# Optimization experiments

Measured on AMD Instinct MI355X. Metric: run time of the kernel, lower is better.

Reference implementation:

```python
import jax, jax.numpy as jnp
import numpy as np

B, L, D = 4, 1024, 256
N_PER, N_HYP = 48, 16  # n_oscillators=64, n_hyperbolic=16
K = N_PER + N_HYP


def _mlp(x, w1, b1, w2, b2):
    # torch nn.Linear: y = x @ W.T + b; GELU is exact (erf) by default
    h = jax.nn.gelu(x @ w1.T + b1, approximate=False)
    return h @ w2.T + b2


def setup_inputs() -> dict:
    key = jax.random.key(0)
    ks = iter(jax.random.split(key, 32))

    def lin(o, i):
        return jax.random.normal(next(ks), (o, i), jnp.float32) * 0.02

    def bias(o):
        return jnp.zeros((o,), jnp.float32)

    inp = {"x": jax.random.normal(next(ks), (B, L, D), jnp.float32)}
    # key/query periodic phase MLPs: Linear(D,D) -> GELU -> Linear(D,N_PER)
    inp.update(kp_w1=lin(D, D), kp_b1=bias(D), kp_w2=lin(N_PER, D), kp_b2=bias(N_PER))
    inp.update(qp_w1=lin(D, D), qp_b1=bias(D), qp_w2=lin(N_PER, D), qp_b2=bias(N_PER))
    # key/query hyperbolic MLPs: Linear(D,D) -> GELU -> Linear(D, 2*N_HYP)
    inp.update(kh_w1=lin(D, D), kh_b1=bias(D), kh_w2=lin(2 * N_HYP, D), kh_b2=bias(2 * N_HYP))
    inp.update(qh_w1=lin(D, D), qh_b1=bias(D), qh_w2=lin(2 * N_HYP, D), qh_b2=bias(2 * N_HYP))
    # value projection and output (LayerNorm + Linear)
    inp.update(v_w=lin(D, D), v_b=bias(D))
    inp.update(ln_g=jnp.ones((D,), jnp.float32), ln_b=jnp.zeros((D,), jnp.float32))
    inp.update(out_w=lin(D, D), out_b=bias(D))
    return inp


def reference(x, kp_w1, kp_b1, kp_w2, kp_b2, qp_w1, qp_b1, qp_w2, qp_b2,
              kh_w1, kh_b1, kh_w2, kh_b2, qh_w1, qh_b1, qh_w2, qh_b2,
              v_w, v_b, ln_g, ln_b, out_w, out_b):
    Bx, Lx, Dx = x.shape

    # periodic (flat torus) phasors: unit-magnitude
    key_p = jnp.tanh(_mlp(x, kp_w1, kp_b1, kp_w2, kp_b2)) * jnp.pi   # (B,L,N_PER)
    query_p = jnp.tanh(_mlp(x, qp_w1, qp_b1, qp_w2, qp_b2)) * jnp.pi
    key_phasor_p = jnp.exp(1j * key_p.astype(jnp.complex64))
    query_phasor_p = jnp.exp(1j * query_p.astype(jnp.complex64))

    # hyperbolic (Poincare-disk) phasors: amplitude = 1 - |z|
    key_h = jnp.tanh(_mlp(x, kh_w1, kh_b1, kh_w2, kh_b2)).reshape(Bx, Lx, N_HYP, 2) * 0.9
    query_h = jnp.tanh(_mlp(x, qh_w1, qh_b1, qh_w2, qh_b2)).reshape(Bx, Lx, N_HYP, 2) * 0.9
    key_ang = jnp.arctan2(key_h[..., 1], key_h[..., 0])
    query_ang = jnp.arctan2(query_h[..., 1], query_h[..., 0])
    key_amp = 1.0 - jnp.sqrt(jnp.sum(key_h * key_h, axis=-1))
    query_amp = 1.0 - jnp.sqrt(jnp.sum(query_h * query_h, axis=-1))
    key_phasor_h = key_amp * jnp.exp(1j * key_ang.astype(jnp.complex64))
    query_phasor_h = query_amp * jnp.exp(1j * query_ang.astype(jnp.complex64))

    key_phasor = jnp.concatenate([key_phasor_p, key_phasor_h], axis=-1)    # (B,L,K)
    query_phasor = jnp.concatenate([query_phasor_p, query_phasor_h], axis=-1)

    V = (x @ v_w.T + v_b).astype(jnp.complex64)                            # (B,L,D)

    # bind: outer product per timestep, cumsum over L (linear-attention scan)
    bound = key_phasor[..., :, None] * V[..., None, :]                     # (B,L,K,D) complex
    memory = jnp.cumsum(bound, axis=1)
    retrieved = jnp.real(jnp.sum(memory * jnp.conj(query_phasor)[..., None], axis=2))  # (B,L,D)

    positions = jnp.arange(1, Lx + 1, dtype=jnp.float32)
    norm = jnp.sqrt(positions * float(K))[None, :, None]
    r = retrieved / norm

    # to_out: LayerNorm(D) -> Linear(D,D)
    mu = jnp.mean(r, axis=-1, keepdims=True)
    var = jnp.mean(jnp.square(r - mu), axis=-1, keepdims=True)
    r_ln = (r - mu) / jnp.sqrt(var + 1e-5) * ln_g + ln_b
    return x + (r_ln @ out_w.T + out_b)
```

## Files before the change

### kernel.cpp

```cpp
#include <hip/hip_runtime.h>
#include <math.h>


#define Bn 4
#define Ln 1024
#define BLn 4096

typedef __attribute__((ext_vector_type(8))) short bf16x8;
typedef __attribute__((ext_vector_type(4))) float f32x4;

__device__ inline ushort f2bf(float f) {
  union { float f; uint u; } x; x.f = f;
  uint r = x.u + 0x7fffu + ((x.u >> 16) & 1u);
  return (ushort)(r >> 16);
}
__device__ inline uint pk2(float a, float b) {
  return (uint)f2bf(a) | ((uint)f2bf(b) << 16);
}

struct G1Prob { const float* X; const float* W; const float* bias; void* Y; int act; };
struct G1Args { G1Prob p[5]; };

__global__ __launch_bounds__(256) void gemm1(G1Args args) {
  const G1Prob p = args.p[blockIdx.z];
  __shared__ ushort As[64 * 40];
  __shared__ ushort Bs[64 * 40];
  const int tid = threadIdx.x;
  const int m0 = blockIdx.x * 64, n0 = blockIdx.y * 64;
  const int lane = tid & 63, wave = tid >> 6;
  const int wr = wave >> 1, wc = wave & 1;
  const int fr = lane & 15, quad = lane >> 4;
  f32x4 acc[2][2];
#pragma unroll
  for (int i = 0; i < 2; i++)
#pragma unroll
    for (int j = 0; j < 2; j++) acc[i][j] = (f32x4){0.f, 0.f, 0.f, 0.f};

  const int srow = tid >> 2, sch = (tid & 3) * 8;
  for (int k0 = 0; k0 < 256; k0 += 32) {
    float4 a0 = *(const float4*)(p.X + (size_t)(m0 + srow) * 256 + k0 + sch);
    float4 a1 = *(const float4*)(p.X + (size_t)(m0 + srow) * 256 + k0 + sch + 4);
    float4 b0 = *(const float4*)(p.W + (size_t)(n0 + srow) * 256 + k0 + sch);
    float4 b1 = *(const float4*)(p.W + (size_t)(n0 + srow) * 256 + k0 + sch + 4);
    uint4 pa = { pk2(a0.x, a0.y), pk2(a0.z, a0.w), pk2(a1.x, a1.y), pk2(a1.z, a1.w) };
    uint4 pb = { pk2(b0.x, b0.y), pk2(b0.z, b0.w), pk2(b1.x, b1.y), pk2(b1.z, b1.w) };
    *(uint4*)&As[srow * 40 + sch] = pa;
    *(uint4*)&Bs[srow * 40 + sch] = pb;
    __syncthreads();
    bf16x8 fa0 = *(const bf16x8*)&As[(wr * 32 + fr) * 40 + quad * 8];
    bf16x8 fa1 = *(const bf16x8*)&As[(wr * 32 + 16 + fr) * 40 + quad * 8];
    bf16x8 fb0 = *(const bf16x8*)&Bs[(wc * 32 + fr) * 40 + quad * 8];
    bf16x8 fb1 = *(const bf16x8*)&Bs[(wc * 32 + 16 + fr) * 40 + quad * 8];
    acc[0][0] = __builtin_amdgcn_mfma_f32_16x16x32_bf16(fa0, fb0, acc[0][0], 0, 0, 0);
    acc[0][1] = __builtin_amdgcn_mfma_f32_16x16x32_bf16(fa0, fb1, acc[0][1], 0, 0, 0);
    acc[1][0] = __builtin_amdgcn_mfma_f32_16x16x32_bf16(fa1, fb0, acc[1][0], 0, 0, 0);
    acc[1][1] = __builtin_amdgcn_mfma_f32_16x16x32_bf16(fa1, fb1, acc[1][1], 0, 0, 0);
    __syncthreads();
  }
#pragma unroll
  for (int i = 0; i < 2; i++)
#pragma unroll
    for (int j = 0; j < 2; j++) {
      int col = n0 + wc * 32 + j * 16 + fr;
      float bv = p.bias[col];
      if (p.act == 4) {
        int rowg0 = m0 + wr * 32 + i * 16 + quad * 4;
        ushort4 st;
        st.x = f2bf(acc[i][j][0] + bv);
        st.y = f2bf(acc[i][j][1] + bv);
        st.z = f2bf(acc[i][j][2] + bv);
        st.w = f2bf(acc[i][j][3] + bv);
        *(ushort4*)((ushort*)p.Y + (size_t)col * 4096 + rowg0) = st;
      } else {
#pragma unroll
        for (int r = 0; r < 4; r++) {
          int rowg = m0 + wr * 32 + i * 16 + quad * 4 + r;
          float o = acc[i][j][r] + bv;
          o = 0.5f * o * (1.0f + erff(o * 0.70710678118654752f));
          ((ushort*)p.Y)[(size_t)rowg * 256 + col] = f2bf(o);
        }
      }
    }
}

struct G2P { const ushort* X; const float* W; const float* bias; uint* Phi;
             int Nreal; float scale; int doT; int isHyp; };
struct G2Args { G2P p[4]; };

__global__ __launch_bounds__(256) void gemm2p(G2Args args, uint* PhiKT) {
  const G2P p = args.p[blockIdx.z];
  __shared__ ushort As[64 * 40];
  __shared__ ushort Bs[64 * 40];
  __shared__ ushort LK[64][130];
  const int tid = threadIdx.x;
  const int m0 = blockIdx.x * 64;
  const int lane = tid & 63, wave = tid >> 6;
  const int wr = wave >> 1, wc = wave & 1;
  const int fr = lane & 15, quad = lane >> 4;
  f32x4 acc[2][2];
#pragma unroll
  for (int i = 0; i < 2; i++)
#pragma unroll
    for (int j = 0; j < 2; j++) acc[i][j] = (f32x4){0.f, 0.f, 0.f, 0.f};

  const int srow = tid >> 2, sch = (tid & 3) * 8;
  for (int k0 = 0; k0 < 256; k0 += 32) {
    uint4 pa = *(const uint4*)(p.X + (size_t)(m0 + srow) * 256 + k0 + sch);
    float4 b0 = {0.f,0.f,0.f,0.f}, b1 = {0.f,0.f,0.f,0.f};
    if (srow < p.Nreal) {
      b0 = *(const float4*)(p.W + (size_t)srow * 256 + k0 + sch);
      b1 = *(const float4*)(p.W + (size_t)srow * 256 + k0 + sch + 4);
    }
    uint4 pb = { pk2(b0.x, b0.y), pk2(b0.z, b0.w), pk2(b1.x, b1.y), pk2(b1.z, b1.w) };
    *(uint4*)&As[srow * 40 + sch] = pa;
    *(uint4*)&Bs[srow * 40 + sch] = pb;
    __syncthreads();
    bf16x8 fa0 = *(const bf16x8*)&As[(wr * 32 + fr) * 40 + quad * 8];
    bf16x8 fa1 = *(const bf16x8*)&As[(wr * 32 + 16 + fr) * 40 + quad * 8];
    bf16x8 fb0 = *(const bf16x8*)&Bs[(wc * 32 + fr) * 40 + quad * 8];
    bf16x8 fb1 = *(const bf16x8*)&Bs[(wc * 32 + 16 + fr) * 40 + quad * 8];
    acc[0][0] = __builtin_amdgcn_mfma_f32_16x16x32_bf16(fa0, fb0, acc[0][0], 0, 0, 0);
    acc[0][1] = __builtin_amdgcn_mfma_f32_16x16x32_bf16(fa0, fb1, acc[0][1], 0, 0, 0);
    acc[1][0] = __builtin_amdgcn_mfma_f32_16x16x32_bf16(fa1, fb0, acc[1][0], 0, 0, 0);
    acc[1][1] = __builtin_amdgcn_mfma_f32_16x16x32_bf16(fa1, fb1, acc[1][1], 0, 0, 0);
    __syncthreads();
  }

#pragma unroll
  for (int i = 0; i < 2; i++)
#pragma unroll
    for (int j = 0; j < 2; j++) {
      int col = wc * 32 + j * 16 + fr;
      float bv = (col < p.Nreal) ? p.bias[col] : 0.f;
#pragma unroll
      for (int r = 0; r < 4; r++) {
        int rowl = wr * 32 + i * 16 + quad * 4 + r;
        int row = m0 + rowl;
        float t = tanhf(acc[i][j][r] + bv) * p.scale;
        if (!p.isHyp) {
          if (col < p.Nreal) {
            float im, re;
            __sincosf(t, &im, &re);
            uint pk = pk2(re, im);
            p.Phi[(size_t)row * 64 + col] = pk;
            if (p.doT) *(uint*)&LK[rowl][2 * col] = pk;
          }
        } else {
          float tp = __shfl_xor(t, 1);
          if ((col & 1) == 0 && col < p.Nreal) {
            float av = t, bw = tp;
            float rr = sqrtf(av * av + bw * bw);
            float re, im;
            if (rr > 0.f) { float inv = (1.0f - rr) / rr; re = av * inv; im = bw * inv; }
            else          { re = 1.0f; im = 0.0f; }
            int k = 48 + (col >> 1);
            uint pk = pk2(re, im);
            p.Phi[(size_t)row * 64 + k] = pk;
            if (p.doT) *(uint*)&LK[rowl][2 * k] = pk;
          }
        }
      }
    }

  if (p.doT) {
    __syncthreads();
    const int b = m0 >> 10, lb0 = m0 & 1023;
    const int nk2 = p.isHyp ? 32 : 96;
    const int k2base = p.isHyp ? 96 : 0;
    const int tot = nk2 * 32;
    for (int idx = tid; idx < tot; idx += 256) {
      int k2 = k2base + (idx >> 5), lp = idx & 31;
      uint v = (uint)LK[lp * 2][k2] | ((uint)LK[lp * 2 + 1][k2] << 16);
      PhiKT[(size_t)b * 65536 + k2 * 512 + (lb0 >> 1) + lp] = v;
    }
  }
}

__global__ __launch_bounds__(256) void kv_prefix(const ushort* VT, const ushort* PhiKT,
                                                 ushort* SpreB) {
  const int b = blockIdx.x >> 4, ds = blockIdx.x & 15;
  const int d0 = ds * 16;
  const int tid = threadIdx.x, lane = tid & 63, wave = tid >> 6;
  const int fr = lane & 15, quad = lane >> 4;
  const int k2b = blockIdx.y * 64 + wave * 16;
  const ushort* pA = PhiKT + (size_t)b * 131072 + (size_t)(k2b + fr) * 1024;
  const ushort* pB = VT + (size_t)(d0 + fr) * 4096 + b * 1024;
  ushort* outp = SpreB + ((size_t)(b * 16) * 256 + d0 + fr) * 128 + k2b + quad * 4;
  f32x4 carry = (f32x4){0.f, 0.f, 0.f, 0.f};
#pragma unroll 4
  for (int c = 0; c < 16; c++) {
    bf16x8 a0 = *(const bf16x8*)(pA + c * 64 + quad * 8);
    bf16x8 b0 = *(const bf16x8*)(pB + c * 64 + quad * 8);
    bf16x8 a1 = *(const bf16x8*)(pA + c * 64 + 32 + quad * 8);
    bf16x8 b1 = *(const bf16x8*)(pB + c * 64 + 32 + quad * 8);
    ushort4 st;
    st.x = f2bf(carry[0]); st.y = f2bf(carry[1]);
    st.z = f2bf(carry[2]); st.w = f2bf(carry[3]);
    *(ushort4*)outp = st;
    outp += 32768;
    f32x4 acc = (f32x4){0.f, 0.f, 0.f, 0.f};
    acc = __builtin_amdgcn_mfma_f32_16x16x32_bf16(a0, b0, acc, 0, 0, 0);
    acc = __builtin_amdgcn_mfma_f32_16x16x32_bf16(a1, b1, acc, 0, 0, 0);
    carry += acc;
  }
}

__global__ __launch_bounds__(256) void retrieve(const ushort* PhiQ, const ushort* PhiK,
                                                const ushort* VT, const ushort* SpreB,
                                                float* R) {
  __shared__ ushort Sl[64 * 72];
  const int bc = blockIdx.x;
  const int b = bc >> 4, c = bc & 15;
  const int d0 = blockIdx.y * 128;
  const int tid = threadIdx.x, lane = tid & 63, wy = tid >> 6;
  const int fr = lane & 15, quad = lane >> 4;
  const int g0 = b * 1024 + c * 64;
  bf16x8 a[4][4];
#pragma unroll
  for (int i = 0; i < 4; i++)
#pragma unroll
    for (int kk = 0; kk < 4; kk++)
      a[i][kk] = *(const bf16x8*)(PhiQ + (size_t)(g0 + i * 16 + fr) * 128 + kk * 32 + quad * 8);

  f32x4 acc[4][2];
#pragma unroll
  for (int i = 0; i < 4; i++)
#pragma unroll
    for (int j = 0; j < 2; j++) acc[i][j] = (f32x4){0.f, 0.f, 0.f, 0.f};

#pragma unroll
  for (int kk = 0; kk < 4; kk++) {
    bf16x8 bb[2];
#pragma unroll
    for (int j = 0; j < 2; j++)
      bb[j] = *(const bf16x8*)(SpreB + ((size_t)bc * 256 + d0 + wy * 32 + j * 16 + fr) * 128 + kk * 32 + quad * 8);
#pragma unroll
    for (int i = 0; i < 4; i++)
#pragma unroll
      for (int j = 0; j < 2; j++)
        acc[i][j] = __builtin_amdgcn_mfma_f32_16x16x32_bf16(a[i][kk], bb[j], acc[i][j], 0, 0, 0);
  }

  f32x4 sacc[4];
#pragma unroll
  for (int i = 0; i < 4; i++) sacc[i] = (f32x4){0.f, 0.f, 0.f, 0.f};
#pragma unroll
  for (int kk = 0; kk < 4; kk++) {
    bf16x8 bs = *(const bf16x8*)(PhiK + (size_t)(g0 + wy * 16 + fr) * 128 + kk * 32 + quad * 8);
#pragma unroll
    for (int i = 0; i < 4; i++)
      sacc[i] = __builtin_amdgcn_mfma_f32_16x16x32_bf16(a[i][kk], bs, sacc[i], 0, 0, 0);
  }
#pragma unroll
  for (int i = 0; i < 4; i++)
#pragma unroll
    for (int r = 0; r < 4; r++) {
      int row = i * 16 + quad * 4 + r;
      int col = wy * 16 + fr;
      Sl[row * 72 + col] = (col <= row) ? f2bf(sacc[i][r]) : (ushort)0;
    }
  __syncthreads();

#pragma unroll
  for (int kk = 0; kk < 2; kk++) {
    bf16x8 as[4], bv[2];
#pragma unroll
    for (int i = 0; i < 4; i++)
      as[i] = *(const bf16x8*)&Sl[(i * 16 + fr) * 72 + kk * 32 + quad * 8];
#pragma unroll
    for (int j = 0; j < 2; j++)
      bv[j] = *(const bf16x8*)(VT + (size_t)(d0 + wy * 32 + j * 16 + fr) * 4096 + g0 + kk * 32 + quad * 8);
#pragma unroll
    for (int i = 0; i < 4; i++)
#pragma unroll
      for (int j = 0; j < 2; j++)
        acc[i][j] = __builtin_amdgcn_mfma_f32_16x16x32_bf16(as[i], bv[j], acc[i][j], 0, 0, 0);
  }

#pragma unroll
  for (int i = 0; i < 4; i++)
#pragma unroll
    for (int j = 0; j < 2; j++)
#pragma unroll
      for (int r = 0; r < 4; r++) {
        int row = i * 16 + quad * 4 + r;
        int d = d0 + wy * 32 + j * 16 + fr;
        float scale = rsqrtf((float)((c * 64 + row + 1) * 64));
        R[(size_t)(g0 + row) * 256 + d] = acc[i][j][r] * scale;
      }
}

__global__ __launch_bounds__(256) void out_ln_gemm(const float* r, const float* g,
                                                   const float* bta, const float* W,
                                                   const float* ob, const float* x,
                                                   float* Y) {
  __shared__ ushort A_lds[64 * 272];
  __shared__ ushort Bs[64 * 40];
  __shared__ float gs[256], bs2[256];
  const int tid = threadIdx.x;
  const int m0 = blockIdx.x * 64, n0 = blockIdx.y * 64;
  gs[tid] = g[tid];
  bs2[tid] = bta[tid];

  const int row_l = tid >> 2, seg = (tid & 3) * 64;
  const float* rr = r + (size_t)(m0 + row_l) * 256 + seg;
  float s = 0.f, sq = 0.f;
#pragma unroll
  for (int i = 0; i < 64; i += 4) {
    float4 v = *(const float4*)(rr + i);
    s += v.x + v.y + v.z + v.w;
    sq += v.x * v.x + v.y * v.y + v.z * v.z + v.w * v.w;
  }
  s += __shfl_xor(s, 1); sq += __shfl_xor(sq, 1);
  s += __shfl_xor(s, 2); sq += __shfl_xor(sq, 2);
  float mean = s * (1.0f / 256.0f);
  float var = fmaxf(sq * (1.0f / 256.0f) - mean * mean, 0.f);
  float rstd = rsqrtf(var + 1e-5f);
  __syncthreads();
#pragma unroll
  for (int i = 0; i < 64; i += 4) {
    float4 v = *(const float4*)(rr + i);
    int k = seg + i;
    ushort4 st;
    st.x = f2bf((v.x - mean) * rstd * gs[k + 0] + bs2[k + 0]);
    st.y = f2bf((v.y - mean) * rstd * gs[k + 1] + bs2[k + 1]);
    st.z = f2bf((v.z - mean) * rstd * gs[k + 2] + bs2[k + 2]);
    st.w = f2bf((v.w - mean) * rstd * gs[k + 3] + bs2[k + 3]);
    *(ushort4*)&A_lds[row_l * 272 + k] = st;
  }
  __syncthreads();

  const int lane = tid & 63, wave = tid >> 6;
  const int wr = wave >> 1, wc = wave & 1;
  const int fr = lane & 15, quad = lane >> 4;
  const int srow = tid >> 2, sch = (tid & 3) * 8;
  f32x4 acc[2][2];
#pragma unroll
  for (int i = 0; i < 2; i++)
#pragma unroll
    for (int j = 0; j < 2; j++) acc[i][j] = (f32x4){0.f, 0.f, 0.f, 0.f};
  for (int k0 = 0; k0 < 256; k0 += 32) {
    float4 b0 = *(const float4*)(W + (size_t)(n0 + srow) * 256 + k0 + sch);
    float4 b1 = *(const float4*)(W + (size_t)(n0 + srow) * 256 + k0 + sch + 4);
    uint4 pb = { pk2(b0.x, b0.y), pk2(b0.z, b0.w), pk2(b1.x, b1.y), pk2(b1.z, b1.w) };
    *(uint4*)&Bs[srow * 40 + sch] = pb;
    __syncthreads();
    bf16x8 fa0 = *(const bf16x8*)&A_lds[(wr * 32 + fr) * 272 + k0 + quad * 8];
    bf16x8 fa1 = *(const bf16x8*)&A_lds[(wr * 32 + 16 + fr) * 272 + k0 + quad * 8];
    bf16x8 fb0 = *(const bf16x8*)&Bs[(wc * 32 + fr) * 40 + quad * 8];
    bf16x8 fb1 = *(const bf16x8*)&Bs[(wc * 32 + 16 + fr) * 40 + quad * 8];
    acc[0][0] = __builtin_amdgcn_mfma_f32_16x16x32_bf16(fa0, fb0, acc[0][0], 0, 0, 0);
    acc[0][1] = __builtin_amdgcn_mfma_f32_16x16x32_bf16(fa0, fb1, acc[0][1], 0, 0, 0);
    acc[1][0] = __builtin_amdgcn_mfma_f32_16x16x32_bf16(fa1, fb0, acc[1][0], 0, 0, 0);
    acc[1][1] = __builtin_amdgcn_mfma_f32_16x16x32_bf16(fa1, fb1, acc[1][1], 0, 0, 0);
    __syncthreads();
  }
#pragma unroll
  for (int i = 0; i < 2; i++)
#pragma unroll
    for (int j = 0; j < 2; j++) {
      int col = n0 + wc * 32 + j * 16 + fr;
      float bv = ob[col];
#pragma unroll
      for (int r = 0; r < 4; r++) {
        int rowg = m0 + wr * 32 + i * 16 + quad * 4 + r;
        Y[(size_t)rowg * 256 + col] = acc[i][j][r] + bv + x[(size_t)rowg * 256 + col];
      }
    }
}

extern "C" void kernel_launch(void* const* d_in, const int* in_sizes, int n_in,
                              void* d_out, int out_size, void* d_ws, size_t ws_size,
                              hipStream_t stream) {
  const float* x     = (const float*)d_in[0];
  const float* kp_w1 = (const float*)d_in[1];
  const float* kp_b1 = (const float*)d_in[2];
  const float* kp_w2 = (const float*)d_in[3];
  const float* kp_b2 = (const float*)d_in[4];
  const float* qp_w1 = (const float*)d_in[5];
  const float* qp_b1 = (const float*)d_in[6];
  const float* qp_w2 = (const float*)d_in[7];
  const float* qp_b2 = (const float*)d_in[8];
  const float* kh_w1 = (const float*)d_in[9];
  const float* kh_b1 = (const float*)d_in[10];
  const float* kh_w2 = (const float*)d_in[11];
  const float* kh_b2 = (const float*)d_in[12];
  const float* qh_w1 = (const float*)d_in[13];
  const float* qh_b1 = (const float*)d_in[14];
  const float* qh_w2 = (const float*)d_in[15];
  const float* qh_b2 = (const float*)d_in[16];
  const float* v_w   = (const float*)d_in[17];
  const float* v_b   = (const float*)d_in[18];
  const float* ln_g  = (const float*)d_in[19];
  const float* ln_b  = (const float*)d_in[20];
  const float* out_w = (const float*)d_in[21];
  const float* out_b = (const float*)d_in[22];

  char* ws = (char*)d_ws;
  const size_t MiB = 1024 * 1024;
  ushort* h0   = (ushort*)(ws + 0);
  ushort* h1   = (ushort*)(ws + 2 * MiB);
  ushort* h2   = (ushort*)(ws + 4 * MiB);
  ushort* h3   = (ushort*)(ws + 6 * MiB);
  ushort* VT   = (ushort*)(ws + 8 * MiB);
  uint*   PhiQ = (uint*)(ws + 10 * MiB);
  uint*   PhiK = (uint*)(ws + 11 * MiB);
  uint*   PhiKT= (uint*)(ws + 12 * MiB);
  ushort* SpreB= (ushort*)(ws + 25 * MiB);
  float*  r    = (float*)(ws + 29 * MiB);

  G1Args g1;
  g1.p[0] = { x, kp_w1, kp_b1, h0, 1 };
  g1.p[1] = { x, qp_w1, qp_b1, h1, 1 };
  g1.p[2] = { x, kh_w1, kh_b1, h2, 1 };
  g1.p[3] = { x, qh_w1, qh_b1, h3, 1 };
  g1.p[4] = { x, v_w,   v_b,   VT, 4 };
  gemm1<<<dim3(64, 4, 5), 256, 0, stream>>>(g1);

  const float PI_F = 3.14159265358979323846f;
  G2Args g2;
  g2.p[0] = { h0, kp_w2, kp_b2, PhiK, 48, PI_F, 1, 0 };
  g2.p[1] = { h1, qp_w2, qp_b2, PhiQ, 48, PI_F, 0, 0 };
  g2.p[2] = { h2, kh_w2, kh_b2, PhiK, 32, 0.9f, 1, 1 };
  g2.p[3] = { h3, qh_w2, qh_b2, PhiQ, 32, 0.9f, 0, 1 };
  gemm2p<<<dim3(64, 1, 4), 256, 0, stream>>>(g2, PhiKT);

  kv_prefix<<<dim3(64, 2), 256, 0, stream>>>(VT, (const ushort*)PhiKT, SpreB);

  retrieve<<<dim3(64, 2), 256, 0, stream>>>((const ushort*)PhiQ, (const ushort*)PhiK,
                                            VT, SpreB, r);

  out_ln_gemm<<<dim3(64, 4), 256, 0, stream>>>(r, ln_g, ln_b, out_w, out_b, x,
                                               (float*)d_out);
}
```

Baseline: 154.7 us.

## Fuse retrieve and LayerNorm-output GEMM into one kernel via LDS

Merges the retrieval kernel and the LayerNorm plus output-projection kernel into a single 512-thread kernel. Each block now covers all 256 channels of a 64-row chunk, keeps the retrieved rows in shared memory, normalizes them there, and runs the output GEMM over the full N=256. This removes one launch and the global round trip of the fp32 intermediate r. In exchange the grid drops to 64 blocks with much more shared memory per block, which lowers parallelism and occupancy on a GPU with many CUs.

```diff
diff --git a/kernel.cpp b/kernel.cpp
--- a/kernel.cpp
+++ b/kernel.cpp
@@ -205,16 +205,22 @@
   }
 }
 
-__global__ __launch_bounds__(256) void retrieve(const ushort* PhiQ, const ushort* PhiK,
-                                                const ushort* VT, const ushort* SpreB,
-                                                float* R) {
+__global__ __launch_bounds__(512) void retrieve_out(
+    const ushort* PhiQ, const ushort* PhiK, const ushort* VT, const ushort* SpreB,
+    const float* g, const float* bta, const float* W, const float* ob,
+    const float* x, float* Y) {
   __shared__ ushort Sl[64 * 72];
+  __shared__ float  rlds[64 * 264];
+  __shared__ ushort A_lds[64 * 272];
+  __shared__ ushort Bs[256 * 40];
+  __shared__ float  gs[256], bs2[256];
   const int bc = blockIdx.x;
-  const int b = bc >> 4, c = bc & 15;
-  const int d0 = blockIdx.y * 128;
-  const int tid = threadIdx.x, lane = tid & 63, wy = tid >> 6;
+  const int c = bc & 15;
+  const int tid = threadIdx.x, lane = tid & 63, w = tid >> 6;
   const int fr = lane & 15, quad = lane >> 4;
-  const int g0 = b * 1024 + c * 64;
+  const int g0 = (bc >> 4) * 1024 + c * 64;
+  if (tid < 256) { gs[tid] = g[tid]; bs2[tid] = bta[tid]; }
+
   bf16x8 a[4][4];
 #pragma unroll
   for (int i = 0; i < 4; i++)
@@ -233,7 +239,7 @@
     bf16x8 bb[2];
 #pragma unroll
     for (int j = 0; j < 2; j++)
-      bb[j] = *(const bf16x8*)(SpreB + ((size_t)bc * 256 + d0 + wy * 32 + j * 16 + fr) * 128 + kk * 32 + quad * 8);
+      bb[j] = *(const bf16x8*)(SpreB + ((size_t)bc * 256 + w * 32 + j * 16 + fr) * 128 + kk * 32 + quad * 8);
 #pragma unroll
     for (int i = 0; i < 4; i++)
 #pragma unroll
@@ -241,24 +247,26 @@
         acc[i][j] = __builtin_amdgcn_mfma_f32_16x16x32_bf16(a[i][kk], bb[j], acc[i][j], 0, 0, 0);
   }
 
-  f32x4 sacc[4];
-#pragma unroll
-  for (int i = 0; i < 4; i++) sacc[i] = (f32x4){0.f, 0.f, 0.f, 0.f};
-#pragma unroll
-  for (int kk = 0; kk < 4; kk++) {
-    bf16x8 bs = *(const bf16x8*)(PhiK + (size_t)(g0 + wy * 16 + fr) * 128 + kk * 32 + quad * 8);
+  if (w < 4) {
+    f32x4 sacc[4];
+#pragma unroll
+    for (int i = 0; i < 4; i++) sacc[i] = (f32x4){0.f, 0.f, 0.f, 0.f};
+#pragma unroll
+    for (int kk = 0; kk < 4; kk++) {
+      bf16x8 bs = *(const bf16x8*)(PhiK + (size_t)(g0 + w * 16 + fr) * 128 + kk * 32 + quad * 8);
+#pragma unroll
+      for (int i = 0; i < 4; i++)
+        sacc[i] = __builtin_amdgcn_mfma_f32_16x16x32_bf16(a[i][kk], bs, sacc[i], 0, 0, 0);
+    }
 #pragma unroll
     for (int i = 0; i < 4; i++)
-      sacc[i] = __builtin_amdgcn_mfma_f32_16x16x32_bf16(a[i][kk], bs, sacc[i], 0, 0, 0);
-  }
-#pragma unroll
-  for (int i = 0; i < 4; i++)
-#pragma unroll
-    for (int r = 0; r < 4; r++) {
-      int row = i * 16 + quad * 4 + r;
-      int col = wy * 16 + fr;
-      Sl[row * 72 + col] = (col <= row) ? f2bf(sacc[i][r]) : (ushort)0;
-    }
+#pragma unroll
+      for (int r = 0; r < 4; r++) {
+        int row = i * 16 + quad * 4 + r;
+        int col = w * 16 + fr;
+        Sl[row * 72 + col] = (col <= row) ? f2bf(sacc[i][r]) : (ushort)0;
+      }
+  }
   __syncthreads();
 
 #pragma unroll
@@ -269,7 +277,7 @@
       as[i] = *(const bf16x8*)&Sl[(i * 16 + fr) * 72 + kk * 32 + quad * 8];
 #pragma unroll
     for (int j = 0; j < 2; j++)
-      bv[j] = *(const bf16x8*)(VT + (size_t)(d0 + wy * 32 + j * 16 + fr) * 4096 + g0 + kk * 32 + quad * 8);
+      bv[j] = *(const bf16x8*)(VT + (size_t)(w * 32 + j * 16 + fr) * 4096 + g0 + kk * 32 + quad * 8);
 #pragma unroll
     for (int i = 0; i < 4; i++)
 #pragma unroll
@@ -284,41 +292,29 @@
 #pragma unroll
       for (int r = 0; r < 4; r++) {
         int row = i * 16 + quad * 4 + r;
-        int d = d0 + wy * 32 + j * 16 + fr;
+        int d = w * 32 + j * 16 + fr;
         float scale = rsqrtf((float)((c * 64 + row + 1) * 64));
-        R[(size_t)(g0 + row) * 256 + d] = acc[i][j][r] * scale;
+        rlds[row * 264 + d] = acc[i][j][r] * scale;
       }
-}
-
-__global__ __launch_bounds__(256) void out_ln_gemm(const float* r, const float* g,
-                                                   const float* bta, const float* W,
-                                                   const float* ob, const float* x,
-                                                   float* Y) {
-  __shared__ ushort A_lds[64 * 272];
-  __shared__ ushort Bs[64 * 40];
-  __shared__ float gs[256], bs2[256];
-  const int tid = threadIdx.x;
-  const int m0 = blockIdx.x * 64, n0 = blockIdx.y * 64;
-  gs[tid] = g[tid];
-  bs2[tid] = bta[tid];
-
-  const int row_l = tid >> 2, seg = (tid & 3) * 64;
-  const float* rr = r + (size_t)(m0 + row_l) * 256 + seg;
+  __syncthreads();
+
+  const int row_l = tid >> 3, seg = (tid & 7) * 32;
+  const float* rr = &rlds[row_l * 264 + seg];
   float s = 0.f, sq = 0.f;
 #pragma unroll
-  for (int i = 0; i < 64; i += 4) {
+  for (int i = 0; i < 32; i += 4) {
     float4 v = *(const float4*)(rr + i);
     s += v.x + v.y + v.z + v.w;
     sq += v.x * v.x + v.y * v.y + v.z * v.z + v.w * v.w;
   }
   s += __shfl_xor(s, 1); sq += __shfl_xor(sq, 1);
   s += __shfl_xor(s, 2); sq += __shfl_xor(sq, 2);
+  s += __shfl_xor(s, 4); sq += __shfl_xor(sq, 4);
   float mean = s * (1.0f / 256.0f);
   float var = fmaxf(sq * (1.0f / 256.0f) - mean * mean, 0.f);
   float rstd = rsqrtf(var + 1e-5f);
-  __syncthreads();
-#pragma unroll
-  for (int i = 0; i < 64; i += 4) {
+#pragma unroll
+  for (int i = 0; i < 32; i += 4) {
     float4 v = *(const float4*)(rr + i);
     int k = seg + i;
     ushort4 st;
@@ -328,43 +324,49 @@
     st.w = f2bf((v.w - mean) * rstd * gs[k + 3] + bs2[k + 3]);
     *(ushort4*)&A_lds[row_l * 272 + k] = st;
   }
-  __syncthreads();
-
-  const int lane = tid & 63, wave = tid >> 6;
-  const int wr = wave >> 1, wc = wave & 1;
-  const int fr = lane & 15, quad = lane >> 4;
-  const int srow = tid >> 2, sch = (tid & 3) * 8;
-  f32x4 acc[2][2];
-#pragma unroll
-  for (int i = 0; i < 2; i++)
-#pragma unroll
-    for (int j = 0; j < 2; j++) acc[i][j] = (f32x4){0.f, 0.f, 0.f, 0.f};
+
+  const int wm = w >> 2, wn = w & 3;
+  f32x4 acc2[2][4];
+#pragma unroll
+  for (int i = 0; i < 2; i++)
+#pragma unroll
+    for (int j = 0; j < 4; j++) acc2[i][j] = (f32x4){0.f, 0.f, 0.f, 0.f};
+
+  const int srow = tid >> 1, sch = (tid & 1) * 16;
   for (int k0 = 0; k0 < 256; k0 += 32) {
-    float4 b0 = *(const float4*)(W + (size_t)(n0 + srow) * 256 + k0 + sch);
-    float4 b1 = *(const float4*)(W + (size_t)(n0 + srow) * 256 + k0 + sch + 4);
-    uint4 pb = { pk2(b0.x, b0.y), pk2(b0.z, b0.w), pk2(b1.x, b1.y), pk2(b1.z, b1.w) };
-    *(uint4*)&Bs[srow * 40 + sch] = pb;
-    __syncthreads();
-    bf16x8 fa0 = *(const bf16x8*)&A_lds[(wr * 32 + fr) * 272 + k0 + quad * 8];
-    bf16x8 fa1 = *(const bf16x8*)&A_lds[(wr * 32 + 16 + fr) * 272 + k0 + quad * 8];
-    bf16x8 fb0 = *(const bf16x8*)&Bs[(wc * 32 + fr) * 40 + quad * 8];
-    bf16x8 fb1 = *(const bf16x8*)&Bs[(wc * 32 + 16 + fr) * 40 + quad * 8];
-    acc[0][0] = __builtin_amdgcn_mfma_f32_16x16x32_bf16(fa0, fb0, acc[0][0], 0, 0, 0);
-    acc[0][1] = __builtin_amdgcn_mfma_f32_16x16x32_bf16(fa0, fb1, acc[0][1], 0, 0, 0);
-    acc[1][0] = __builtin_amdgcn_mfma_f32_16x16x32_bf16(fa1, fb0, acc[1][0], 0, 0, 0);
-    acc[1][1] = __builtin_amdgcn_mfma_f32_16x16x32_bf16(fa1, fb1, acc[1][1], 0, 0, 0);
-    __syncthreads();
-  }
-#pragma unroll
-  for (int i = 0; i < 2; i++)
-#pragma unroll
-    for (int j = 0; j < 2; j++) {
-      int col = n0 + wc * 32 + j * 16 + fr;
+    float4 b0 = *(const float4*)(W + (size_t)srow * 256 + k0 + sch);
+    float4 b1 = *(const float4*)(W + (size_t)srow * 256 + k0 + sch + 4);
+    float4 b2 = *(const float4*)(W + (size_t)srow * 256 + k0 + sch + 8);
+    float4 b3 = *(const float4*)(W + (size_t)srow * 256 + k0 + sch + 12);
+    uint4 p0 = { pk2(b0.x, b0.y), pk2(b0.z, b0.w), pk2(b1.x, b1.y), pk2(b1.z, b1.w) };
+    uint4 p1 = { pk2(b2.x, b2.y), pk2(b2.z, b2.w), pk2(b3.x, b3.y), pk2(b3.z, b3.w) };
+    *(uint4*)&Bs[srow * 40 + sch] = p0;
+    *(uint4*)&Bs[srow * 40 + sch + 8] = p1;
+    __syncthreads();
+    bf16x8 fa[2], fb[4];
+#pragma unroll
+    for (int i = 0; i < 2; i++)
+      fa[i] = *(const bf16x8*)&A_lds[(wm * 32 + i * 16 + fr) * 272 + k0 + quad * 8];
+#pragma unroll
+    for (int j = 0; j < 4; j++)
+      fb[j] = *(const bf16x8*)&Bs[(wn * 64 + j * 16 + fr) * 40 + quad * 8];
+#pragma unroll
+    for (int i = 0; i < 2; i++)
+#pragma unroll
+      for (int j = 0; j < 4; j++)
+        acc2[i][j] = __builtin_amdgcn_mfma_f32_16x16x32_bf16(fa[i], fb[j], acc2[i][j], 0, 0, 0);
+    __syncthreads();
+  }
+#pragma unroll
+  for (int i = 0; i < 2; i++)
+#pragma unroll
+    for (int j = 0; j < 4; j++) {
+      int col = wn * 64 + j * 16 + fr;
       float bv = ob[col];
 #pragma unroll
       for (int r = 0; r < 4; r++) {
-        int rowg = m0 + wr * 32 + i * 16 + quad * 4 + r;
-        Y[(size_t)rowg * 256 + col] = acc[i][j][r] + bv + x[(size_t)rowg * 256 + col];
+        int rowg = g0 + wm * 32 + i * 16 + quad * 4 + r;
+        Y[(size_t)rowg * 256 + col] = acc2[i][j][r] + bv + x[(size_t)rowg * 256 + col];
       }
     }
 }
@@ -407,7 +409,6 @@
   uint*   PhiK = (uint*)(ws + 11 * MiB);
   uint*   PhiKT= (uint*)(ws + 12 * MiB);
   ushort* SpreB= (ushort*)(ws + 25 * MiB);
-  float*  r    = (float*)(ws + 29 * MiB);
 
   G1Args g1;
   g1.p[0] = { x, kp_w1, kp_b1, h0, 1 };
@@ -427,9 +428,7 @@
 
   kv_prefix<<<dim3(64, 2), 256, 0, stream>>>(VT, (const ushort*)PhiKT, SpreB);
 
-  retrieve<<<dim3(64, 2), 256, 0, stream>>>((const ushort*)PhiQ, (const ushort*)PhiK,
-                                            VT, SpreB, r);
-
-  out_ln_gemm<<<dim3(64, 4), 256, 0, stream>>>(r, ln_g, ln_b, out_w, out_b, x,
-                                               (float*)d_out);
-}
+  retrieve_out<<<dim3(64), 512, 0, stream>>>((const ushort*)PhiQ, (const ushort*)PhiK,
+                                             VT, SpreB, ln_g, ln_b, out_w, out_b, x,
+                                             (float*)d_out);
+}
```

Result: slower. 159.0 us (+2.8%).
